# Kernel tuning notes

Measured on AMD Instinct MI355X. Metric: run time of the kernel, lower is better.

The kernel has to match this reference:

```python
import jax, jax.numpy as jnp
import numpy as np

B, S, D, H = 2, 2048, 1024, 16
HD = D // H  # head_dim = 64
NEG = -100000.0  # matches torch masked_fill value


def setup_inputs() -> dict:
    key = jax.random.key(0)
    ks = jax.random.split(key, 8)
    return {
        "queries": jax.random.normal(ks[0], (B, S, D), jnp.float32),
        "keys": jax.random.normal(ks[1], (B, S, D), jnp.float32),
        "values": jax.random.normal(ks[2], (B, S, D), jnp.float32),
        "mask": jax.random.randint(ks[3], (B, S), 0, 2, jnp.int32),
        # torch nn.Linear weights are [out_features, in_features]
        "Wq": jax.random.normal(ks[4], (D, D), jnp.float32) / np.sqrt(D),
        "Wk": jax.random.normal(ks[5], (D, D), jnp.float32) / np.sqrt(D),
        "Wv": jax.random.normal(ks[6], (D, D), jnp.float32) / np.sqrt(D),
        "Wo": jax.random.normal(ks[7], (D, D), jnp.float32) / np.sqrt(D),
    }


def reference(queries, keys, values, mask, Wq, Wk, Wv, Wo):
    b, lq, _ = queries.shape
    # projections (Linear: x @ W.T), split heads -> [b, h, s, hd]
    q = (queries @ Wq.T).reshape(b, lq, H, HD).transpose(0, 2, 1, 3)
    k = (keys @ Wk.T).reshape(b, -1, H, HD).transpose(0, 2, 1, 3)
    v = (values @ Wv.T).reshape(b, -1, H, HD).transpose(0, 2, 1, 3)
    # scaled dot-product attention with padding mask on key positions
    scores = jnp.einsum("bhqd,bhkd->bhqk", q, k) / jnp.sqrt(jnp.float32(HD))
    m = (mask[:, None, None, :] != 0)  # [b,1,1,lk] broadcast over heads, queries
    scores = jnp.where(m, scores, NEG)
    w = jax.nn.softmax(scores, axis=-1)
    w = jnp.where(m, w, 0.0)
    out = jnp.einsum("bhqk,bhkd->bhqd", w, v)
    out = out.transpose(0, 2, 1, 3).reshape(b, lq, H * HD)
    return out @ Wo.T
```

## Files before the change

kernel.cpp:

```cpp
#include <hip/hip_runtime.h>
#include <hip/hip_bf16.h>
#include <type_traits>
#include <cmath>

#define B_ 2
#define S_ 2048
#define D_ 1024
#define H_ 16
#define HD_ 64

typedef __attribute__((ext_vector_type(8))) short bf16x8;
typedef __attribute__((ext_vector_type(4))) float f32x4;

#define GLOAD_LDS16(gp, lp)                                      \
  __builtin_amdgcn_global_load_lds(                              \
      (const __attribute__((address_space(1))) void*)(gp),       \
      (__attribute__((address_space(3))) void*)(lp), 16, 0, 0)

__device__ __forceinline__ short f2bf_s(float x) {
  __hip_bfloat16 h = __float2bfloat16(x);
  return *reinterpret_cast<short*>(&h);
}
__device__ __forceinline__ unsigned f2bf_u(float x) {
  __hip_bfloat16 h = __float2bfloat16(x);
  return (unsigned)*reinterpret_cast<unsigned short*>(&h);
}

__global__ __launch_bounds__(256) void cvt_all(
    const float* __restrict__ q, const float* __restrict__ k, const float* __restrict__ v,
    const float* __restrict__ wq, const float* __restrict__ wk,
    const float* __restrict__ wv, const float* __restrict__ wo,
    __hip_bfloat16* __restrict__ qb, __hip_bfloat16* __restrict__ kb, __hip_bfloat16* __restrict__ vb,
    __hip_bfloat16* __restrict__ wqb, __hip_bfloat16* __restrict__ wkb,
    __hip_bfloat16* __restrict__ wvb, __hip_bfloat16* __restrict__ wob) {
  size_t t = (size_t)blockIdx.x * 256 + threadIdx.x;
  const float* s;
  __hip_bfloat16* d;
  size_t off;
  if (t < (size_t)3 << 19) {
    size_t which = t >> 19;
    off = (t & ((1u << 19) - 1)) << 3;
    s = which == 0 ? q : which == 1 ? k : v;
    d = which == 0 ? qb : which == 1 ? kb : vb;
  } else {
    size_t u = t - ((size_t)3 << 19);
    size_t which = u >> 17;
    off = (u & ((1u << 17) - 1)) << 3;
    s = which == 0 ? wq : which == 1 ? wk : which == 2 ? wv : wo;
    d = which == 0 ? wqb : which == 1 ? wkb : which == 2 ? wvb : wob;
  }
  float4 a = *reinterpret_cast<const float4*>(s + off);
  float4 b = *reinterpret_cast<const float4*>(s + off + 4);
  bf16x8 r;
  r[0] = f2bf_s(a.x); r[1] = f2bf_s(a.y); r[2] = f2bf_s(a.z); r[3] = f2bf_s(a.w);
  r[4] = f2bf_s(b.x); r[5] = f2bf_s(b.y); r[6] = f2bf_s(b.z); r[7] = f2bf_s(b.w);
  *reinterpret_cast<bf16x8*>(d + off) = r;
}

__global__ __launch_bounds__(256) void transpose_v(const __hip_bfloat16* __restrict__ Vp,
                                                   __hip_bfloat16* __restrict__ Vt) {
  __shared__ __hip_bfloat16 T[64][72];
  const int s0 = blockIdx.x * 64;
  const int h = blockIdx.y;
  const int b = blockIdx.z;
  const int tid = threadIdx.x;
  const int r = tid >> 3;
  const int c = (tid & 7) * 8;
#pragma unroll
  for (int i = 0; i < 2; ++i) {
    int row = r + i * 32;
    *reinterpret_cast<bf16x8*>(&T[row][c]) =
        *reinterpret_cast<const bf16x8*>(Vp + ((size_t)(b * S_ + s0 + row)) * D_ + h * HD_ + c);
  }
  __syncthreads();
#pragma unroll
  for (int i = 0; i < 2; ++i) {
    int dd = r + i * 32;
    alignas(16) __hip_bfloat16 tmp[8];
#pragma unroll
    for (int j = 0; j < 8; ++j) tmp[j] = T[c + j][dd];
    *reinterpret_cast<bf16x8*>(Vt + ((size_t)((b * H_ + h) * HD_ + dd)) * S_ + s0 + c) =
        *reinterpret_cast<const bf16x8*>(tmp);
  }
}

template <typename OT>
__global__ __launch_bounds__(256) void gemm3_bt(
    const __hip_bfloat16* __restrict__ A0, const __hip_bfloat16* __restrict__ A1,
    const __hip_bfloat16* __restrict__ A2,
    const __hip_bfloat16* __restrict__ Bt0, const __hip_bfloat16* __restrict__ Bt1,
    const __hip_bfloat16* __restrict__ Bt2,
    OT* __restrict__ C0, OT* __restrict__ C1, OT* __restrict__ C2,
    int M, int N, int K) {
  __shared__ __hip_bfloat16 As[128 * 32];
  __shared__ __hip_bfloat16 Bs[128 * 32];
  const int z = blockIdx.z;
  const __hip_bfloat16* A = z == 0 ? A0 : z == 1 ? A1 : A2;
  const __hip_bfloat16* Bt = z == 0 ? Bt0 : z == 1 ? Bt1 : Bt2;
  OT* C = z == 0 ? C0 : z == 1 ? C1 : C2;

  const int tid = threadIdx.x;
  const int lane = tid & 63;
  const int w = tid >> 6;
  const int wr = w >> 1, wc = w & 1;
  const int lr = lane & 15;
  const int lg = lane >> 4;
  const int m0 = blockIdx.y * 128, n0 = blockIdx.x * 128;

  const int srow = w * 16 + (lane >> 2);
  const int scol = (lane & 3) * 8;
  const __hip_bfloat16* aS = A + (size_t)(m0 + srow) * K + scol;
  const __hip_bfloat16* bS = Bt + (size_t)(n0 + srow) * K + scol;
  char* lA = (char*)As + w * 1024;
  char* lB = (char*)Bs + w * 1024;

  f32x4 acc[4][4] = {};

  for (int k0 = 0; k0 < K; k0 += 32) {
    __syncthreads();
    GLOAD_LDS16(aS + k0, lA);
    GLOAD_LDS16(aS + (size_t)64 * K + k0, lA + 4096);
    GLOAD_LDS16(bS + k0, lB);
    GLOAD_LDS16(bS + (size_t)64 * K + k0, lB + 4096);
    __syncthreads();

    bf16x8 af[4], bfr[4];
#pragma unroll
    for (int mi = 0; mi < 4; ++mi)
      af[mi] = *reinterpret_cast<const bf16x8*>((char*)As + (wr * 64 + mi * 16 + lr) * 64 + lg * 16);
#pragma unroll
    for (int ni = 0; ni < 4; ++ni)
      bfr[ni] = *reinterpret_cast<const bf16x8*>((char*)Bs + (wc * 64 + ni * 16 + lr) * 64 + lg * 16);
#pragma unroll
    for (int mi = 0; mi < 4; ++mi)
#pragma unroll
      for (int ni = 0; ni < 4; ++ni)
        acc[mi][ni] = __builtin_amdgcn_mfma_f32_16x16x32_bf16(af[mi], bfr[ni], acc[mi][ni], 0, 0, 0);
  }

#pragma unroll
  for (int mi = 0; mi < 4; ++mi)
#pragma unroll
    for (int ni = 0; ni < 4; ++ni)
#pragma unroll
      for (int r = 0; r < 4; ++r) {
        int row = m0 + wr * 64 + mi * 16 + lg * 4 + r;
        int col = n0 + wc * 64 + ni * 16 + lr;
        if constexpr (std::is_same<OT, float>::value)
          C[(size_t)row * N + col] = acc[mi][ni][r];
        else
          C[(size_t)row * N + col] = __float2bfloat16(acc[mi][ni][r]);
      }
}

__global__ __launch_bounds__(256) void attn_fwd2(const __hip_bfloat16* __restrict__ Qp,
                                                 const __hip_bfloat16* __restrict__ Kp,
                                                 const __hip_bfloat16* __restrict__ Vt,
                                                 const int* __restrict__ mask,
                                                 __hip_bfloat16* __restrict__ ctx) {
  __shared__ __hip_bfloat16 Ks[64 * 64];
  __shared__ __hip_bfloat16 Vs[64 * 64];
  __shared__ __hip_bfloat16 Ps[4][16 * 64];
  __shared__ alignas(16) float smask[64];

  const int tid = threadIdx.x;
  const int lane = tid & 63;
  const int w = tid >> 6;
  const int lr = lane & 15;
  const int lg = lane >> 4;
  const int q0 = blockIdx.x * 64;
  const int h = blockIdx.y;
  const int b = blockIdx.z;

  const size_t qoff = ((size_t)(b * S_ + q0 + w * 16 + lr)) * D_ + h * HD_;
  const bf16x8 qf0 = *reinterpret_cast<const bf16x8*>(Qp + qoff + lg * 8);
  const bf16x8 qf1 = *reinterpret_cast<const bf16x8*>(Qp + qoff + 32 + lg * 8);

  f32x4 acco[4] = {};
  float m_run = -60000.f, l_run = 0.f;

  const int srow = w * 8 + (lane >> 3);
  const int sc = lane & 7;
  const int sj = sc ^ (srow & 7);
  const __hip_bfloat16* kbase = Kp + ((size_t)(b * S_)) * D_ + h * HD_;
  const __hip_bfloat16* vbase = Vt + ((size_t)((b * H_ + h) * HD_)) * S_;
  char* ldsK = (char*)Ks + w * 1024;
  char* ldsV = (char*)Vs + w * 1024;
  char* pw = (char*)&Ps[w][0];

  const float C_SC = 0.18033688011f;

  for (int kt = 0; kt < S_ / 64; ++kt) {
    const int kv0 = kt * 64;
    __syncthreads();
    GLOAD_LDS16(kbase + (size_t)(kv0 + srow) * D_ + sj * 8, ldsK);
    GLOAD_LDS16(kbase + (size_t)(kv0 + 32 + srow) * D_ + sj * 8, ldsK + 4096);
    GLOAD_LDS16(vbase + (size_t)srow * S_ + kv0 + sj * 8, ldsV);
    GLOAD_LDS16(vbase + (size_t)(32 + srow) * S_ + kv0 + sj * 8, ldsV + 4096);
    if (tid < 64) smask[tid] = (mask[b * S_ + kv0 + tid] != 0) ? 0.f : -60000.f;
    __syncthreads();

    f32x4 accs[4];
#pragma unroll
    for (int kb = 0; kb < 4; ++kb) {
      const int row = kb * 16 + lr;
      const int sw = lr & 7;
      bf16x8 k0 = *reinterpret_cast<const bf16x8*>((char*)Ks + row * 128 + (((0 + lg) ^ sw) << 4));
      bf16x8 k1 = *reinterpret_cast<const bf16x8*>((char*)Ks + row * 128 + (((4 + lg) ^ sw) << 4));
      f32x4 a = {};
      a = __builtin_amdgcn_mfma_f32_16x16x32_bf16(k0, qf0, a, 0, 0, 0);
      a = __builtin_amdgcn_mfma_f32_16x16x32_bf16(k1, qf1, a, 0, 0, 0);
      accs[kb] = a;
    }

#pragma unroll
    for (int kb = 0; kb < 4; ++kb) {
      float4 bias = *reinterpret_cast<const float4*>(&smask[kb * 16 + lg * 4]);
      accs[kb][0] = fmaf(accs[kb][0], C_SC, bias.x);
      accs[kb][1] = fmaf(accs[kb][1], C_SC, bias.y);
      accs[kb][2] = fmaf(accs[kb][2], C_SC, bias.z);
      accs[kb][3] = fmaf(accs[kb][3], C_SC, bias.w);
    }

    float mx = accs[0][0];
#pragma unroll
    for (int kb = 0; kb < 4; ++kb)
#pragma unroll
      for (int r = 0; r < 4; ++r) mx = fmaxf(mx, accs[kb][r]);
    mx = fmaxf(mx, __shfl_xor(mx, 16));
    mx = fmaxf(mx, __shfl_xor(mx, 32));
    const float mn = fmaxf(m_run, mx);
    const float scale = exp2f(m_run - mn);
    m_run = mn;
    float rs = 0.f;
#pragma unroll
    for (int kb = 0; kb < 4; ++kb)
#pragma unroll
      for (int r = 0; r < 4; ++r) {
        accs[kb][r] = exp2f(accs[kb][r] - mn);
        rs += accs[kb][r];
      }
    rs += __shfl_xor(rs, 16);
    rs += __shfl_xor(rs, 32);
    l_run = l_run * scale + rs;

#pragma unroll
    for (int kb = 0; kb < 4; ++kb)
#pragma unroll
      for (int i = 0; i < 2; ++i) {
        unsigned pk = f2bf_u(accs[kb][2 * i]) | (f2bf_u(accs[kb][2 * i + 1]) << 16);
        const int off = kb * 32 + lg * 8 + i * 4;
        const int fin = lr * 128 + ((((off >> 4) ^ (lr & 7))) << 4) + (off & 15);
        *reinterpret_cast<unsigned*>(pw + fin) = pk;
      }

    float sc_r[4];
#pragma unroll
    for (int r = 0; r < 4; ++r) sc_r[r] = __shfl(scale, (lane & 48) | (lg * 4 + r));
#pragma unroll
    for (int nb = 0; nb < 4; ++nb)
#pragma unroll
      for (int r = 0; r < 4; ++r) acco[nb][r] *= sc_r[r];

#pragma unroll
    for (int win = 0; win < 2; ++win) {
      bf16x8 pa = *reinterpret_cast<const bf16x8*>(
          pw + lr * 128 + ((((win * 4 + lg) ^ (lr & 7))) << 4));
#pragma unroll
      for (int nb = 0; nb < 4; ++nb) {
        const int row = nb * 16 + lr;
        bf16x8 vb = *reinterpret_cast<const bf16x8*>(
            (char*)Vs + row * 128 + ((((win * 4 + lg) ^ (lr & 7))) << 4));
        acco[nb] = __builtin_amdgcn_mfma_f32_16x16x32_bf16(pa, vb, acco[nb], 0, 0, 0);
      }
    }
  }

  float linv[4];
#pragma unroll
  for (int r = 0; r < 4; ++r) {
    float lv = __shfl(l_run, (lane & 48) | (lg * 4 + r));
    linv[r] = 1.f / lv;
  }
#pragma unroll
  for (int nb = 0; nb < 4; ++nb)
#pragma unroll
    for (int r = 0; r < 4; ++r) {
      int q = q0 + w * 16 + lg * 4 + r;
      ctx[((size_t)(b * S_ + q)) * D_ + h * HD_ + nb * 16 + lr] =
          __float2bfloat16(acco[nb][r] * linv[r]);
    }
}

extern "C" void kernel_launch(void* const* d_in, const int* in_sizes, int n_in,
                              void* d_out, int out_size, void* d_ws, size_t ws_size,
                              hipStream_t stream) {
  const float* queries = (const float*)d_in[0];
  const float* keys    = (const float*)d_in[1];
  const float* values  = (const float*)d_in[2];
  const int*   mask    = (const int*)d_in[3];
  const float* Wq      = (const float*)d_in[4];
  const float* Wk      = (const float*)d_in[5];
  const float* Wv      = (const float*)d_in[6];
  const float* Wo      = (const float*)d_in[7];

  const size_t NT = (size_t)B_ * S_ * D_;
  const size_t NW = (size_t)D_ * D_;
  __hip_bfloat16* ws = reinterpret_cast<__hip_bfloat16*>(d_ws);
  __hip_bfloat16* qb  = ws;
  __hip_bfloat16* kb  = ws + NT;
  __hip_bfloat16* vb  = ws + 2 * NT;
  __hip_bfloat16* wqb = ws + 3 * NT;
  __hip_bfloat16* wkb = wqb + NW;
  __hip_bfloat16* wvb = wkb + NW;
  __hip_bfloat16* wob = wvb + NW;
  __hip_bfloat16* Qp  = wob + NW;
  __hip_bfloat16* Kp  = Qp + NT;
  __hip_bfloat16* Vp  = Kp + NT;
  __hip_bfloat16* Vtr = qb;
  __hip_bfloat16* ctx = kb;

  const int M = B_ * S_;

  cvt_all<<<8192, 256, 0, stream>>>(queries, keys, values, Wq, Wk, Wv, Wo,
                                    qb, kb, vb, wqb, wkb, wvb, wob);
  gemm3_bt<__hip_bfloat16><<<dim3(D_ / 128, M / 128, 3), 256, 0, stream>>>(
      qb, kb, vb, wqb, wkb, wvb, Qp, Kp, Vp, M, D_, D_);
  transpose_v<<<dim3(S_ / 64, H_, B_), 256, 0, stream>>>(Vp, Vtr);
  attn_fwd2<<<dim3(S_ / 64, H_, B_), 256, 0, stream>>>(Qp, Kp, Vtr, mask, ctx);
  gemm3_bt<float><<<dim3(D_ / 128, M / 128, 1), 256, 0, stream>>>(
      ctx, ctx, ctx, wob, wob, wob, (float*)d_out, (float*)d_out, (float*)d_out, M, D_, D_);
}
```

Measured before the change: 274.3 us.

## Fold mask and scale into inputs, fuse V transpose, enlarge attention KV tile

Folds the softmax scale into Wq during conversion and zeroes masked rows of the value input, so the attention kernel no longer applies a bias. The row sum is computed by an MFMA against a bf16 mask vector. The V projection GEMM now writes head-transposed output directly, which removes the separate transpose kernel. The attention kernel processes 128-key tiles and rescales only when the running max grows by more than 8 (lazy rescaling). Masked keys no longer get -inf scores, so they still enter the max computation; this risks precision changes, while the removed launches and per-tile softmax work should save time.

```diff
diff --git a/kernel.cpp b/kernel.cpp
--- a/kernel.cpp
+++ b/kernel.cpp
@@ -1,7 +1,6 @@
 #include <hip/hip_runtime.h>
 #include <hip/hip_bf16.h>
 #include <type_traits>
-#include <cmath>
 
 #define B_ 2
 #define S_ 2048
@@ -17,6 +16,8 @@
       (const __attribute__((address_space(1))) void*)(gp),       \
       (__attribute__((address_space(3))) void*)(lp), 16, 0, 0)
 
+#define MFMA16(a, b, c) __builtin_amdgcn_mfma_f32_16x16x32_bf16((a), (b), (c), 0, 0, 0)
+
 __device__ __forceinline__ short f2bf_s(float x) {
   __hip_bfloat16 h = __float2bfloat16(x);
   return *reinterpret_cast<short*>(&h);
@@ -28,59 +29,49 @@
 
 __global__ __launch_bounds__(256) void cvt_all(
     const float* __restrict__ q, const float* __restrict__ k, const float* __restrict__ v,
+    const int* __restrict__ mask,
     const float* __restrict__ wq, const float* __restrict__ wk,
     const float* __restrict__ wv, const float* __restrict__ wo,
     __hip_bfloat16* __restrict__ qb, __hip_bfloat16* __restrict__ kb, __hip_bfloat16* __restrict__ vb,
     __hip_bfloat16* __restrict__ wqb, __hip_bfloat16* __restrict__ wkb,
-    __hip_bfloat16* __restrict__ wvb, __hip_bfloat16* __restrict__ wob) {
+    __hip_bfloat16* __restrict__ wvb, __hip_bfloat16* __restrict__ wob,
+    __hip_bfloat16* __restrict__ maskb) {
+  const float C_SC = 0.18033688011112042f;
   size_t t = (size_t)blockIdx.x * 256 + threadIdx.x;
-  const float* s;
-  __hip_bfloat16* d;
-  size_t off;
-  if (t < (size_t)3 << 19) {
+  if (t < ((size_t)3 << 19)) {
     size_t which = t >> 19;
-    off = (t & ((1u << 19) - 1)) << 3;
-    s = which == 0 ? q : which == 1 ? k : v;
-    d = which == 0 ? qb : which == 1 ? kb : vb;
-  } else {
+    size_t off = (t & (((size_t)1 << 19) - 1)) << 3;
+    const float* s = which == 0 ? q : which == 1 ? k : v;
+    __hip_bfloat16* d = which == 0 ? qb : which == 1 ? kb : vb;
+    float4 a = *reinterpret_cast<const float4*>(s + off);
+    float4 bv = *reinterpret_cast<const float4*>(s + off + 4);
+    bf16x8 r;
+    r[0] = f2bf_s(a.x);  r[1] = f2bf_s(a.y);  r[2] = f2bf_s(a.z);  r[3] = f2bf_s(a.w);
+    r[4] = f2bf_s(bv.x); r[5] = f2bf_s(bv.y); r[6] = f2bf_s(bv.z); r[7] = f2bf_s(bv.w);
+    if (which == 2) {
+      if (mask[off >> 10] == 0) {
+        bf16x8 z = {0, 0, 0, 0, 0, 0, 0, 0};
+        r = z;
+      }
+    }
+    *reinterpret_cast<bf16x8*>(d + off) = r;
+  } else if (t < ((size_t)1 << 21)) {
     size_t u = t - ((size_t)3 << 19);
     size_t which = u >> 17;
-    off = (u & ((1u << 17) - 1)) << 3;
-    s = which == 0 ? wq : which == 1 ? wk : which == 2 ? wv : wo;
-    d = which == 0 ? wqb : which == 1 ? wkb : which == 2 ? wvb : wob;
-  }
-  float4 a = *reinterpret_cast<const float4*>(s + off);
-  float4 b = *reinterpret_cast<const float4*>(s + off + 4);
-  bf16x8 r;
-  r[0] = f2bf_s(a.x); r[1] = f2bf_s(a.y); r[2] = f2bf_s(a.z); r[3] = f2bf_s(a.w);
-  r[4] = f2bf_s(b.x); r[5] = f2bf_s(b.y); r[6] = f2bf_s(b.z); r[7] = f2bf_s(b.w);
-  *reinterpret_cast<bf16x8*>(d + off) = r;
-}
-
-__global__ __launch_bounds__(256) void transpose_v(const __hip_bfloat16* __restrict__ Vp,
-                                                   __hip_bfloat16* __restrict__ Vt) {
-  __shared__ __hip_bfloat16 T[64][72];
-  const int s0 = blockIdx.x * 64;
-  const int h = blockIdx.y;
-  const int b = blockIdx.z;
-  const int tid = threadIdx.x;
-  const int r = tid >> 3;
-  const int c = (tid & 7) * 8;
-#pragma unroll
-  for (int i = 0; i < 2; ++i) {
-    int row = r + i * 32;
-    *reinterpret_cast<bf16x8*>(&T[row][c]) =
-        *reinterpret_cast<const bf16x8*>(Vp + ((size_t)(b * S_ + s0 + row)) * D_ + h * HD_ + c);
-  }
-  __syncthreads();
-#pragma unroll
-  for (int i = 0; i < 2; ++i) {
-    int dd = r + i * 32;
-    alignas(16) __hip_bfloat16 tmp[8];
-#pragma unroll
-    for (int j = 0; j < 8; ++j) tmp[j] = T[c + j][dd];
-    *reinterpret_cast<bf16x8*>(Vt + ((size_t)((b * H_ + h) * HD_ + dd)) * S_ + s0 + c) =
-        *reinterpret_cast<const bf16x8*>(tmp);
+    size_t off = (u & (((size_t)1 << 17) - 1)) << 3;
+    const float* s = which == 0 ? wq : which == 1 ? wk : which == 2 ? wv : wo;
+    __hip_bfloat16* d = which == 0 ? wqb : which == 1 ? wkb : which == 2 ? wvb : wob;
+    const float sc = (which == 0) ? C_SC : 1.0f;
+    float4 a = *reinterpret_cast<const float4*>(s + off);
+    float4 bv = *reinterpret_cast<const float4*>(s + off + 4);
+    bf16x8 r;
+    r[0] = f2bf_s(a.x * sc);  r[1] = f2bf_s(a.y * sc);  r[2] = f2bf_s(a.z * sc);  r[3] = f2bf_s(a.w * sc);
+    r[4] = f2bf_s(bv.x * sc); r[5] = f2bf_s(bv.y * sc); r[6] = f2bf_s(bv.z * sc); r[7] = f2bf_s(bv.w * sc);
+    *reinterpret_cast<bf16x8*>(d + off) = r;
+  } else {
+    int idx = (int)(t - ((size_t)1 << 21));
+    unsigned short o = mask[idx] ? (unsigned short)0x3F80 : (unsigned short)0;
+    maskb[idx] = *reinterpret_cast<__hip_bfloat16*>(&o);
   }
 }
 
@@ -135,7 +126,31 @@
     for (int mi = 0; mi < 4; ++mi)
 #pragma unroll
       for (int ni = 0; ni < 4; ++ni)
-        acc[mi][ni] = __builtin_amdgcn_mfma_f32_16x16x32_bf16(af[mi], bfr[ni], acc[mi][ni], 0, 0, 0);
+        acc[mi][ni] = MFMA16(af[mi], bfr[ni], acc[mi][ni]);
+  }
+
+  if constexpr (std::is_same<OT, __hip_bfloat16>::value) {
+    if (z == 2) {
+#pragma unroll
+      for (int mi = 0; mi < 4; ++mi) {
+        const int row = m0 + wr * 64 + mi * 16 + lg * 4;
+        const int bb = row >> 11;
+        const int ss = row & (S_ - 1);
+#pragma unroll
+        for (int ni = 0; ni < 4; ++ni) {
+          const int col = n0 + wc * 64 + ni * 16 + lr;
+          const int hh = col >> 6, dd = col & 63;
+          short4 pk;
+          pk.x = f2bf_s(acc[mi][ni][0]);
+          pk.y = f2bf_s(acc[mi][ni][1]);
+          pk.z = f2bf_s(acc[mi][ni][2]);
+          pk.w = f2bf_s(acc[mi][ni][3]);
+          *reinterpret_cast<short4*>(
+              (__hip_bfloat16*)C + ((size_t)((bb * H_ + hh) * HD_ + dd)) * S_ + ss) = pk;
+        }
+      }
+      return;
+    }
   }
 
 #pragma unroll
@@ -153,15 +168,15 @@
       }
 }
 
-__global__ __launch_bounds__(256) void attn_fwd2(const __hip_bfloat16* __restrict__ Qp,
-                                                 const __hip_bfloat16* __restrict__ Kp,
-                                                 const __hip_bfloat16* __restrict__ Vt,
-                                                 const int* __restrict__ mask,
-                                                 __hip_bfloat16* __restrict__ ctx) {
-  __shared__ __hip_bfloat16 Ks[64 * 64];
-  __shared__ __hip_bfloat16 Vs[64 * 64];
+__global__ __launch_bounds__(256, 4) void attn_fwd3(
+    const __hip_bfloat16* __restrict__ Qp,
+    const __hip_bfloat16* __restrict__ Kp,
+    const __hip_bfloat16* __restrict__ Vt,
+    const __hip_bfloat16* __restrict__ maskb,
+    __hip_bfloat16* __restrict__ ctx) {
+  __shared__ __hip_bfloat16 Ks[128 * 64];
+  __shared__ __hip_bfloat16 Vs[64 * 128];
   __shared__ __hip_bfloat16 Ps[4][16 * 64];
-  __shared__ alignas(16) float smask[64];
 
   const int tid = threadIdx.x;
   const int lane = tid & 63;
@@ -177,117 +192,109 @@
   const bf16x8 qf1 = *reinterpret_cast<const bf16x8*>(Qp + qoff + 32 + lg * 8);
 
   f32x4 acco[4] = {};
-  float m_run = -60000.f, l_run = 0.f;
-
-  const int srow = w * 8 + (lane >> 3);
-  const int sc = lane & 7;
-  const int sj = sc ^ (srow & 7);
+  f32x4 accl = {};
+  float m_run = 0.f;
+
+  const int krow_in = lane >> 3;
+  const int sjk = (lane & 7) ^ krow_in;
+  const int vrow_in = lane >> 4;
   const __hip_bfloat16* kbase = Kp + ((size_t)(b * S_)) * D_ + h * HD_;
   const __hip_bfloat16* vbase = Vt + ((size_t)((b * H_ + h) * HD_)) * S_;
-  char* ldsK = (char*)Ks + w * 1024;
-  char* ldsV = (char*)Vs + w * 1024;
+  const __hip_bfloat16* mbase = maskb + b * S_;
   char* pw = (char*)&Ps[w][0];
-
-  const float C_SC = 0.18033688011f;
-
-  for (int kt = 0; kt < S_ / 64; ++kt) {
-    const int kv0 = kt * 64;
+  const int sw = lr & 7;
+
+  for (int kt = 0; kt < S_ / 128; ++kt) {
+    const int kv0 = kt * 128;
     __syncthreads();
-    GLOAD_LDS16(kbase + (size_t)(kv0 + srow) * D_ + sj * 8, ldsK);
-    GLOAD_LDS16(kbase + (size_t)(kv0 + 32 + srow) * D_ + sj * 8, ldsK + 4096);
-    GLOAD_LDS16(vbase + (size_t)srow * S_ + kv0 + sj * 8, ldsV);
-    GLOAD_LDS16(vbase + (size_t)(32 + srow) * S_ + kv0 + sj * 8, ldsV + 4096);
-    if (tid < 64) smask[tid] = (mask[b * S_ + kv0 + tid] != 0) ? 0.f : -60000.f;
+#pragma unroll
+    for (int i = 0; i < 4; ++i) {
+      const int j = w * 4 + i;
+      GLOAD_LDS16(kbase + (size_t)(kv0 + 8 * j + krow_in) * D_ + sjk * 8,
+                  (char*)Ks + j * 1024);
+      const int vrow = 4 * j + vrow_in;
+      const int sjv = (lane & 15) ^ ((((j & 1) << 2)) | vrow_in);
+      GLOAD_LDS16(vbase + (size_t)vrow * S_ + kv0 + sjv * 8,
+                  (char*)Vs + j * 1024);
+    }
+    bf16x8 mfr[4];
+#pragma unroll
+    for (int ks = 0; ks < 4; ++ks)
+      mfr[ks] = *reinterpret_cast<const bf16x8*>(mbase + kv0 + ks * 32 + lg * 8);
     __syncthreads();
 
-    f32x4 accs[4];
-#pragma unroll
-    for (int kb = 0; kb < 4; ++kb) {
+    f32x4 accs[8];
+#pragma unroll
+    for (int kb = 0; kb < 8; ++kb) {
       const int row = kb * 16 + lr;
-      const int sw = lr & 7;
-      bf16x8 k0 = *reinterpret_cast<const bf16x8*>((char*)Ks + row * 128 + (((0 + lg) ^ sw) << 4));
+      bf16x8 k0 = *reinterpret_cast<const bf16x8*>((char*)Ks + row * 128 + ((lg ^ sw) << 4));
       bf16x8 k1 = *reinterpret_cast<const bf16x8*>((char*)Ks + row * 128 + (((4 + lg) ^ sw) << 4));
       f32x4 a = {};
-      a = __builtin_amdgcn_mfma_f32_16x16x32_bf16(k0, qf0, a, 0, 0, 0);
-      a = __builtin_amdgcn_mfma_f32_16x16x32_bf16(k1, qf1, a, 0, 0, 0);
+      a = MFMA16(k0, qf0, a);
+      a = MFMA16(k1, qf1, a);
       accs[kb] = a;
     }
 
-#pragma unroll
-    for (int kb = 0; kb < 4; ++kb) {
-      float4 bias = *reinterpret_cast<const float4*>(&smask[kb * 16 + lg * 4]);
-      accs[kb][0] = fmaf(accs[kb][0], C_SC, bias.x);
-      accs[kb][1] = fmaf(accs[kb][1], C_SC, bias.y);
-      accs[kb][2] = fmaf(accs[kb][2], C_SC, bias.z);
-      accs[kb][3] = fmaf(accs[kb][3], C_SC, bias.w);
-    }
-
-    float mx = accs[0][0];
-#pragma unroll
-    for (int kb = 0; kb < 4; ++kb)
-#pragma unroll
-      for (int r = 0; r < 4; ++r) mx = fmaxf(mx, accs[kb][r]);
+    float mx = fmaxf(fmaxf(accs[0][0], accs[0][1]), fmaxf(accs[0][2], accs[0][3]));
+#pragma unroll
+    for (int kb = 1; kb < 8; ++kb)
+      mx = fmaxf(mx, fmaxf(fmaxf(accs[kb][0], accs[kb][1]), fmaxf(accs[kb][2], accs[kb][3])));
     mx = fmaxf(mx, __shfl_xor(mx, 16));
     mx = fmaxf(mx, __shfl_xor(mx, 32));
-    const float mn = fmaxf(m_run, mx);
-    const float scale = exp2f(m_run - mn);
-    m_run = mn;
-    float rs = 0.f;
-#pragma unroll
-    for (int kb = 0; kb < 4; ++kb)
+
+    if (__ballot(mx > m_run + 8.f) != 0ULL) {
+      const float mn = fmaxf(m_run, mx);
+      const float sc = exp2f(m_run - mn);
+      m_run = mn;
 #pragma unroll
       for (int r = 0; r < 4; ++r) {
-        accs[kb][r] = exp2f(accs[kb][r] - mn);
-        rs += accs[kb][r];
-      }
-    rs += __shfl_xor(rs, 16);
-    rs += __shfl_xor(rs, 32);
-    l_run = l_run * scale + rs;
-
-#pragma unroll
-    for (int kb = 0; kb < 4; ++kb)
-#pragma unroll
-      for (int i = 0; i < 2; ++i) {
-        unsigned pk = f2bf_u(accs[kb][2 * i]) | (f2bf_u(accs[kb][2 * i + 1]) << 16);
-        const int off = kb * 32 + lg * 8 + i * 4;
-        const int fin = lr * 128 + ((((off >> 4) ^ (lr & 7))) << 4) + (off & 15);
-        *reinterpret_cast<unsigned*>(pw + fin) = pk;
-      }
-
-    float sc_r[4];
-#pragma unroll
-    for (int r = 0; r < 4; ++r) sc_r[r] = __shfl(scale, (lane & 48) | (lg * 4 + r));
-#pragma unroll
-    for (int nb = 0; nb < 4; ++nb)
-#pragma unroll
-      for (int r = 0; r < 4; ++r) acco[nb][r] *= sc_r[r];
-
-#pragma unroll
-    for (int win = 0; win < 2; ++win) {
-      bf16x8 pa = *reinterpret_cast<const bf16x8*>(
-          pw + lr * 128 + ((((win * 4 + lg) ^ (lr & 7))) << 4));
-#pragma unroll
-      for (int nb = 0; nb < 4; ++nb) {
-        const int row = nb * 16 + lr;
-        bf16x8 vb = *reinterpret_cast<const bf16x8*>(
-            (char*)Vs + row * 128 + ((((win * 4 + lg) ^ (lr & 7))) << 4));
-        acco[nb] = __builtin_amdgcn_mfma_f32_16x16x32_bf16(pa, vb, acco[nb], 0, 0, 0);
+        const float s = __shfl(sc, (lane & 48) | (lg * 4 + r));
+        acco[0][r] *= s; acco[1][r] *= s; acco[2][r] *= s; acco[3][r] *= s;
+        accl[r] *= s;
+      }
+    }
+
+#pragma unroll
+    for (int half = 0; half < 2; ++half) {
+#pragma unroll
+      for (int kb2 = 0; kb2 < 4; ++kb2) {
+        const int kb = half * 4 + kb2;
+#pragma unroll
+        for (int r = 0; r < 4; ++r) accs[kb][r] = exp2f(accs[kb][r] - m_run);
+#pragma unroll
+        for (int i = 0; i < 2; ++i) {
+          unsigned pk = f2bf_u(accs[kb][2 * i]) | (f2bf_u(accs[kb][2 * i + 1]) << 16);
+          const int off = kb2 * 32 + lg * 8 + i * 4;
+          const int fin = lr * 128 + ((((off >> 4) ^ sw)) << 4) + (off & 15);
+          *reinterpret_cast<unsigned*>(pw + fin) = pk;
+        }
+      }
+#pragma unroll
+      for (int ks2 = 0; ks2 < 2; ++ks2) {
+        const int ks = half * 2 + ks2;
+        bf16x8 pa = *reinterpret_cast<const bf16x8*>(
+            pw + lr * 128 + ((((ks2 * 4 + lg) ^ sw)) << 4));
+        accl = MFMA16(pa, mfr[ks], accl);
+#pragma unroll
+        for (int nb = 0; nb < 4; ++nb) {
+          const int row = nb * 16 + lr;
+          bf16x8 vbf = *reinterpret_cast<const bf16x8*>(
+              (char*)Vs + row * 256 + ((((ks * 4 + lg) ^ sw)) << 4));
+          acco[nb] = MFMA16(pa, vbf, acco[nb]);
+        }
       }
     }
   }
 
-  float linv[4];
-#pragma unroll
-  for (int r = 0; r < 4; ++r) {
-    float lv = __shfl(l_run, (lane & 48) | (lg * 4 + r));
-    linv[r] = 1.f / lv;
-  }
+  f32x4 linv;
+#pragma unroll
+  for (int r = 0; r < 4; ++r) linv[r] = 1.f / accl[r];
 #pragma unroll
   for (int nb = 0; nb < 4; ++nb)
 #pragma unroll
     for (int r = 0; r < 4; ++r) {
-      int q = q0 + w * 16 + lg * 4 + r;
-      ctx[((size_t)(b * S_ + q)) * D_ + h * HD_ + nb * 16 + lr] =
+      const int qq = q0 + w * 16 + lg * 4 + r;
+      ctx[((size_t)(b * S_ + qq)) * D_ + h * HD_ + nb * 16 + lr] =
           __float2bfloat16(acco[nb][r] * linv[r]);
     }
 }
@@ -307,27 +314,26 @@
   const size_t NT = (size_t)B_ * S_ * D_;
   const size_t NW = (size_t)D_ * D_;
   __hip_bfloat16* ws = reinterpret_cast<__hip_bfloat16*>(d_ws);
-  __hip_bfloat16* qb  = ws;
-  __hip_bfloat16* kb  = ws + NT;
-  __hip_bfloat16* vb  = ws + 2 * NT;
-  __hip_bfloat16* wqb = ws + 3 * NT;
-  __hip_bfloat16* wkb = wqb + NW;
-  __hip_bfloat16* wvb = wkb + NW;
-  __hip_bfloat16* wob = wvb + NW;
-  __hip_bfloat16* Qp  = wob + NW;
-  __hip_bfloat16* Kp  = Qp + NT;
-  __hip_bfloat16* Vp  = Kp + NT;
-  __hip_bfloat16* Vtr = qb;
-  __hip_bfloat16* ctx = kb;
+  __hip_bfloat16* qb    = ws;
+  __hip_bfloat16* kb    = ws + NT;
+  __hip_bfloat16* vb    = ws + 2 * NT;
+  __hip_bfloat16* wqb   = ws + 3 * NT;
+  __hip_bfloat16* wkb   = wqb + NW;
+  __hip_bfloat16* wvb   = wkb + NW;
+  __hip_bfloat16* wob   = wvb + NW;
+  __hip_bfloat16* maskb = wob + NW;
+  __hip_bfloat16* Qp    = maskb + 4096;
+  __hip_bfloat16* Kp    = Qp + NT;
+  __hip_bfloat16* Vtp   = Kp + NT;
+  __hip_bfloat16* ctx   = kb;
 
   const int M = B_ * S_;
 
-  cvt_all<<<8192, 256, 0, stream>>>(queries, keys, values, Wq, Wk, Wv, Wo,
-                                    qb, kb, vb, wqb, wkb, wvb, wob);
+  cvt_all<<<8208, 256, 0, stream>>>(queries, keys, values, mask, Wq, Wk, Wv, Wo,
+                                    qb, kb, vb, wqb, wkb, wvb, wob, maskb);
   gemm3_bt<__hip_bfloat16><<<dim3(D_ / 128, M / 128, 3), 256, 0, stream>>>(
-      qb, kb, vb, wqb, wkb, wvb, Qp, Kp, Vp, M, D_, D_);
-  transpose_v<<<dim3(S_ / 64, H_, B_), 256, 0, stream>>>(Vp, Vtr);
-  attn_fwd2<<<dim3(S_ / 64, H_, B_), 256, 0, stream>>>(Qp, Kp, Vtr, mask, ctx);
+      qb, kb, vb, wqb, wkb, wvb, Qp, Kp, Vtp, M, D_, D_);
+  attn_fwd3<<<dim3(S_ / 64, H_, B_), 256, 0, stream>>>(Qp, Kp, Vtp, maskb, ctx);
   gemm3_bt<float><<<dim3(D_ / 128, M / 128, 1), 256, 0, stream>>>(
       ctx, ctx, ctx, wob, wob, wob, (float*)d_out, (float*)d_out, (float*)d_out, M, D_, D_);
 }
```

After: 252.4 us. 1.09x faster.
